# Kernel optimization log

Measured on AMD Instinct MI355X. Metric: run time of the kernel, lower is better.

The kernel has to match this reference:

```python
import jax, jax.numpy as jnp
import numpy as np

B, S, E, H = 2, 2048, 1024, 16
D = E // H  # head dim = 64


def setup_inputs() -> dict:
    key = jax.random.key(0)
    k1, k2, k3 = jax.random.split(key, 3)
    x = jax.random.normal(k1, (B, S, E), dtype=jnp.float32)
    W_attn = jax.random.normal(k2, (E, 3 * E), dtype=jnp.float32) * (1.0 / np.sqrt(E))
    b_attn = jnp.zeros((3 * E,), dtype=jnp.float32)
    W_proj = jax.random.normal(k3, (E, E), dtype=jnp.float32) * (1.0 / np.sqrt(E))
    b_proj = jnp.zeros((E,), dtype=jnp.float32)
    return {"x": x, "W_attn": W_attn, "b_attn": b_attn, "W_proj": W_proj, "b_proj": b_proj}


def reference(x, W_attn, b_attn, W_proj, b_proj):
    b, s, e = x.shape
    qkv = x @ W_attn + b_attn                      # (B, S, 3E)
    q, k, v = jnp.split(qkv, 3, axis=-1)
    # (B, S, E) -> (B, H, S, D)
    def heads(t):
        return t.reshape(b, s, H, D).transpose(0, 2, 1, 3)
    q, k, v = heads(q), heads(k), heads(v)
    scale = 1.0 / np.sqrt(D)
    # ring QK^T over world_size=1 == full QK^T; scores (B, H, S, S)
    attn = jnp.einsum("bhqd,bhkd->bhqk", q, k) * scale
    causal = jnp.tril(jnp.ones((s, s), dtype=bool))
    attn = jnp.where(causal[None, None], attn, -jnp.inf)
    attn = jax.nn.softmax(attn, axis=-1)
    # ring AV over world_size=1 == full AV
    y = jnp.einsum("bhqk,bhkd->bhqd", attn, v)     # (B, H, S, D)
    y = y.transpose(0, 2, 1, 3).reshape(b, s, e)   # (B, S, E)
    return y @ W_proj + b_proj
```

## Files before the change

### kernel.cpp

```cpp
#include <hip/hip_runtime.h>
#include <hip/hip_bf16.h>

#define B_ 2
#define S_ 2048
#define E_ 1024
#define H_ 16
#define D_ 64

typedef __attribute__((ext_vector_type(8))) _Float16 half8;
typedef __attribute__((ext_vector_type(4))) _Float16 half4;
typedef __attribute__((ext_vector_type(4))) float floatx4;

__device__ inline void gload16(const _Float16* g, _Float16* l) {
    __builtin_amdgcn_global_load_lds(
        (const __attribute__((address_space(1))) void*)g,
        (__attribute__((address_space(3))) void*)l, 16, 0, 0);
}

__global__ __launch_bounds__(256) void k_cvt(const float* __restrict__ in,
                                             _Float16* __restrict__ out, int n) {
    int i = (blockIdx.x * 256 + threadIdx.x) * 8;
    if (i >= n) return;
    float4 a = *(const float4*)(in + i);
    float4 b = *(const float4*)(in + i + 4);
    half8 o;
    o[0] = (_Float16)a.x; o[1] = (_Float16)a.y; o[2] = (_Float16)a.z; o[3] = (_Float16)a.w;
    o[4] = (_Float16)b.x; o[5] = (_Float16)b.y; o[6] = (_Float16)b.z; o[7] = (_Float16)b.w;
    *(half8*)(out + i) = o;
}

__global__ __launch_bounds__(256) void k_transpose_cvt(const float* __restrict__ in,
                                                       _Float16* __restrict__ out, int R, int C) {
    __shared__ _Float16 tile[32][33];
    int tx = threadIdx.x & 31, ty = threadIdx.x >> 5;
    int c0 = blockIdx.x * 32, r0 = blockIdx.y * 32;
#pragma unroll
    for (int k = 0; k < 4; k++) {
        int r = ty + k * 8;
        tile[r][tx] = (_Float16)in[(size_t)(r0 + r) * C + c0 + tx];
    }
    __syncthreads();
#pragma unroll
    for (int k = 0; k < 4; k++) {
        int r = ty + k * 8;
        out[(size_t)(c0 + r) * R + r0 + tx] = tile[tx][r];
    }
}

template <int MODE>
__global__ __launch_bounds__(256) void k_gemm(const _Float16* __restrict__ A,
                                              const _Float16* __restrict__ Bt,
                                              const float* __restrict__ bias,
                                              void* __restrict__ out0,
                                              _Float16* __restrict__ out1,
                                              _Float16* __restrict__ out2,
                                              int M, int N, int K) {
    __shared__ __align__(16) _Float16 As[128 * 32];
    __shared__ __align__(16) _Float16 Bs[128 * 32];
    int tid = threadIdx.x;
    int lane = tid & 63, w = tid >> 6;
    int wm = w >> 1, wn = w & 1;
    int l15 = lane & 15, quad = lane >> 4;
    int m0 = blockIdx.y * 128, n0 = blockIdx.x * 128;

    floatx4 acc[4][4];
    floatx4 zero = {0.f, 0.f, 0.f, 0.f};
#pragma unroll
    for (int i = 0; i < 4; i++)
#pragma unroll
        for (int j = 0; j < 4; j++) acc[i][j] = zero;

    for (int k0 = 0; k0 < K; k0 += 32) {
        __syncthreads();
#pragma unroll
        for (int c = 0; c < 2; c++) {
            int flat = c * 2048 + tid * 8;
            int row = flat >> 5, col = flat & 31;
            gload16(A + (size_t)(m0 + row) * K + k0 + col, &As[c * 2048 + w * 512]);
            gload16(Bt + (size_t)(n0 + row) * K + k0 + col, &Bs[c * 2048 + w * 512]);
        }
        __syncthreads();
        half8 af[4], bfr[4];
#pragma unroll
        for (int i = 0; i < 4; i++) af[i] = *(const half8*)&As[(wm * 64 + i * 16 + l15) * 32 + quad * 8];
#pragma unroll
        for (int j = 0; j < 4; j++) bfr[j] = *(const half8*)&Bs[(wn * 64 + j * 16 + l15) * 32 + quad * 8];
#pragma unroll
        for (int i = 0; i < 4; i++)
#pragma unroll
            for (int j = 0; j < 4; j++)
                acc[i][j] = __builtin_amdgcn_mfma_f32_16x16x32_f16(af[i], bfr[j], acc[i][j], 0, 0, 0);
    }
#pragma unroll
    for (int j = 0; j < 4; j++) {
        int gcol = n0 + wn * 64 + j * 16 + l15;
        float bj = bias[gcol];
        int sect = gcol >> 10, e = gcol & 1023;
        int hh = e >> 6, dd = e & 63;
#pragma unroll
        for (int i = 0; i < 4; i++) {
            int grow = m0 + wm * 64 + i * 16 + quad * 4;
#pragma unroll
            for (int r = 0; r < 4; r++) {
                float v = acc[i][j][r] + bj;
                if (MODE == 1) {
                    ((float*)out0)[(size_t)(grow + r) * N + gcol] = v;
                } else {
                    int row = grow + r;
                    int bb = row >> 11, ss = row & 2047;
                    size_t hb = (size_t)(bb * H_ + hh);
                    _Float16 v16 = (_Float16)v;
                    if (sect == 0)
                        ((_Float16*)out0)[(hb * S_ + ss) * D_ + dd] = v16;
                    else if (sect == 1)
                        out1[(hb * S_ + ss) * D_ + dd] = v16;
                    else
                        out2[(hb * D_ + dd) * S_ + ss] = v16;
                }
            }
        }
    }
}

__global__ __launch_bounds__(256) __attribute__((amdgpu_waves_per_eu(2, 4)))
void k_attn(const _Float16* __restrict__ Qh,
            const _Float16* __restrict__ Kh,
            const _Float16* __restrict__ Vt,
            _Float16* __restrict__ y) {
    __shared__ __align__(16) _Float16 smem_h[25600];
    int tid = threadIdx.x;
    int lane = tid & 63, w = tid >> 6;
    int l15 = lane & 15, quad = lane >> 4;
    _Float16* KsB = smem_h;
    _Float16* VsB = smem_h + 8192;
    _Float16* Pw = smem_h + 16384 + w * 2304;

    int bidx = blockIdx.x;
    int bh = 4 * (bidx & 7) + ((bidx >> 3) & 3);
    int qidx = (bidx >> 5) & 7;
    int qb = (bidx >> 8) ? qidx : (15 - qidx);
    int b = bh >> 4, h = bh & 15;

    const size_t hbase = (size_t)bh * (S_ * D_);
    const _Float16* Qp = Qh + hbase;
    const _Float16* Kp = Kh + hbase;
    const _Float16* Vp = Vt + hbase;

    int q0w = qb * 128 + 32 * w;
    int ktd = q0w >> 6;
    int ktmax = 2 * qb + 1;

    int r0 = tid >> 3;
    int cbh = ((tid * 8) & 63) ^ ((r0 & 7) << 3);
    const _Float16* kS0 = Kp + (size_t)r0 * D_ + cbh;
    const _Float16* kS1 = Kp + (size_t)(r0 + 32) * D_ + cbh;
    const _Float16* vS0 = Vp + (size_t)r0 * S_ + cbh;
    const _Float16* vS1 = Vp + (size_t)(r0 + 32) * S_ + cbh;

#define STAGE(kt_, buf_)                                              \
    do {                                                              \
        gload16(kS0 + (kt_) * 4096, KsB + (buf_) * 4096 + w * 512);   \
        gload16(kS1 + (kt_) * 4096, KsB + (buf_) * 4096 + 2048 + w * 512); \
        gload16(vS0 + (kt_) * 64, VsB + (buf_) * 4096 + w * 512);     \
        gload16(vS1 + (kt_) * 64, VsB + (buf_) * 4096 + 2048 + w * 512); \
    } while (0)

    half8 aq[2][2];
#pragma unroll
    for (int i = 0; i < 2; i++)
#pragma unroll
        for (int kk = 0; kk < 2; kk++) {
            half8 q = *(const half8*)(Qp + (size_t)(q0w + i * 16 + l15) * D_ + kk * 32 + quad * 8);
#pragma unroll
            for (int u = 0; u < 8; u++) q[u] *= (_Float16)0.125f;
            aq[i][kk] = q;
        }

    floatx4 zero = {0.f, 0.f, 0.f, 0.f};
    floatx4 o[2][4];
#pragma unroll
    for (int i = 0; i < 2; i++)
#pragma unroll
        for (int f = 0; f < 4; f++) o[i][f] = zero;
    float l_run[2] = {0.f, 0.f};

    STAGE(0, 0);
    int cur = 0;
    int swz = (l15 & 7) << 3;
    for (int kt = 0; kt <= ktmax; kt++) {
        __syncthreads();
        if (kt < ktmax) STAGE(kt + 1, cur ^ 1);
        if (kt <= ktd) {
            const _Float16* KC = KsB + cur * 4096;
            const _Float16* VC = VsB + cur * 4096;
            floatx4 sa[2][4];
#pragma unroll
            for (int jj = 0; jj < 4; jj++) {
                int row = jj * 16 + l15;
                half8 k0 = *(const half8*)&KC[row * 64 + ((quad * 8) ^ swz)];
                half8 k1 = *(const half8*)&KC[row * 64 + ((32 + quad * 8) ^ swz)];
#pragma unroll
                for (int i = 0; i < 2; i++) {
                    floatx4 a = zero;
                    a = __builtin_amdgcn_mfma_f32_16x16x32_f16(k0, aq[i][0], a, 0, 0, 0);
                    a = __builtin_amdgcn_mfma_f32_16x16x32_f16(k1, aq[i][1], a, 0, 0, 0);
                    sa[i][jj] = a;
                }
            }
            bool diag = (kt == ktd);
            int k64 = kt * 64;
#pragma unroll
            for (int i = 0; i < 2; i++) {
                float ssum = 0.f;
#pragma unroll
                for (int jj = 0; jj < 4; jj++) {
                    half4 pk;
#pragma unroll
                    for (int r = 0; r < 4; r++) {
                        float v = __expf(sa[i][jj][r]);
                        if (diag) {
                            int key = k64 + jj * 16 + quad * 4 + r;
                            int query = q0w + i * 16 + l15;
                            if (key > query) v = 0.f;
                        }
                        ssum += v;
                        pk[r] = (_Float16)v;
                    }
                    *(half4*)&Pw[(i * 16 + l15) * 72 + jj * 16 + quad * 4] = pk;
                }
                ssum += __shfl_xor(ssum, 16);
                ssum += __shfl_xor(ssum, 32);
                l_run[i] += ssum;
            }
#pragma unroll
            for (int kk = 0; kk < 2; kk++) {
                half8 ap0 = *(const half8*)&Pw[(0 * 16 + l15) * 72 + kk * 32 + quad * 8];
                half8 ap1 = *(const half8*)&Pw[(1 * 16 + l15) * 72 + kk * 32 + quad * 8];
#pragma unroll
                for (int f = 0; f < 4; f++) {
                    int row = f * 16 + l15;
                    half8 bv = *(const half8*)&VC[row * 64 + ((kk * 32 + quad * 8) ^ swz)];
                    o[0][f] = __builtin_amdgcn_mfma_f32_16x16x32_f16(ap0, bv, o[0][f], 0, 0, 0);
                    o[1][f] = __builtin_amdgcn_mfma_f32_16x16x32_f16(ap1, bv, o[1][f], 0, 0, 0);
                }
            }
        }
        cur ^= 1;
    }
#undef STAGE

#pragma unroll
    for (int i = 0; i < 2; i++) {
        float linv[4];
#pragma unroll
        for (int r = 0; r < 4; r++) linv[r] = 1.0f / __shfl(l_run[i], quad * 4 + r);
#pragma unroll
        for (int f = 0; f < 4; f++)
#pragma unroll
            for (int r = 0; r < 4; r++) {
                int row = q0w + i * 16 + quad * 4 + r;
                y[((size_t)(b * S_ + row)) * E_ + h * D_ + f * 16 + l15] =
                    (_Float16)(o[i][f][r] * linv[r]);
            }
    }
}

extern "C" void kernel_launch(void* const* d_in, const int* in_sizes, int n_in,
                              void* d_out, int out_size, void* d_ws, size_t ws_size,
                              hipStream_t stream) {
    const float* x      = (const float*)d_in[0];
    const float* W_attn = (const float*)d_in[1];
    const float* b_attn = (const float*)d_in[2];
    const float* W_proj = (const float*)d_in[3];
    const float* b_proj = (const float*)d_in[4];
    float* out = (float*)d_out;

    const int M = B_ * S_;
    char* ws = (char*)d_ws;
    _Float16* xh  = (_Float16*)ws; ws += (size_t)M * E_ * 2;
    _Float16* Wat = (_Float16*)ws; ws += (size_t)3 * E_ * E_ * 2;
    _Float16* Wpt = (_Float16*)ws; ws += (size_t)E_ * E_ * 2;
    _Float16* Qh  = (_Float16*)ws; ws += (size_t)M * E_ * 2;
    _Float16* Kh  = (_Float16*)ws; ws += (size_t)M * E_ * 2;
    _Float16* Vt  = (_Float16*)ws; ws += (size_t)M * E_ * 2;
    _Float16* yh  = xh;

    k_cvt<<<(M * E_) / 2048, 256, 0, stream>>>(x, xh, M * E_);
    k_transpose_cvt<<<dim3(3 * E_ / 32, E_ / 32), 256, 0, stream>>>(W_attn, Wat, E_, 3 * E_);
    k_transpose_cvt<<<dim3(E_ / 32, E_ / 32), 256, 0, stream>>>(W_proj, Wpt, E_, E_);

    k_gemm<0><<<dim3(3 * E_ / 128, M / 128), 256, 0, stream>>>(xh, Wat, b_attn, Qh, Kh, Vt, M, 3 * E_, E_);
    k_attn<<<512, 256, 0, stream>>>(Qh, Kh, Vt, yh);
    k_gemm<1><<<dim3(E_ / 128, M / 128), 256, 0, stream>>>(yh, Wpt, b_proj, (void*)out, nullptr, nullptr, M, E_, E_);
}
```

Before: 201.9 us.

## Use 8 waves per attention block and merge prep conversions into one kernel

```diff
diff --git a/kernel.cpp b/kernel.cpp
--- a/kernel.cpp
+++ b/kernel.cpp
@@ -17,23 +17,35 @@
         (__attribute__((address_space(3))) void*)l, 16, 0, 0);
 }
 
-__global__ __launch_bounds__(256) void k_cvt(const float* __restrict__ in,
-                                             _Float16* __restrict__ out, int n) {
-    int i = (blockIdx.x * 256 + threadIdx.x) * 8;
-    if (i >= n) return;
-    float4 a = *(const float4*)(in + i);
-    float4 b = *(const float4*)(in + i + 4);
-    half8 o;
-    o[0] = (_Float16)a.x; o[1] = (_Float16)a.y; o[2] = (_Float16)a.z; o[3] = (_Float16)a.w;
-    o[4] = (_Float16)b.x; o[5] = (_Float16)b.y; o[6] = (_Float16)b.z; o[7] = (_Float16)b.w;
-    *(half8*)(out + i) = o;
-}
-
-__global__ __launch_bounds__(256) void k_transpose_cvt(const float* __restrict__ in,
-                                                       _Float16* __restrict__ out, int R, int C) {
+__global__ __launch_bounds__(256) void k_prep(const float* __restrict__ x, _Float16* __restrict__ xh,
+                                              const float* __restrict__ Wa, _Float16* __restrict__ Wat,
+                                              const float* __restrict__ Wp, _Float16* __restrict__ Wpt) {
     __shared__ _Float16 tile[32][33];
-    int tx = threadIdx.x & 31, ty = threadIdx.x >> 5;
-    int c0 = blockIdx.x * 32, r0 = blockIdx.y * 32;
+    int bid = blockIdx.x, tid = threadIdx.x;
+    if (bid < 2048) {
+        int i = (bid * 256 + tid) * 8;
+        float4 a = *(const float4*)(x + i);
+        float4 b = *(const float4*)(x + i + 4);
+        half8 o;
+        o[0] = (_Float16)a.x; o[1] = (_Float16)a.y; o[2] = (_Float16)a.z; o[3] = (_Float16)a.w;
+        o[4] = (_Float16)b.x; o[5] = (_Float16)b.y; o[6] = (_Float16)b.z; o[7] = (_Float16)b.w;
+        *(half8*)(xh + i) = o;
+        return;
+    }
+    const float* in;
+    _Float16* out;
+    int R, C, bx, by;
+    if (bid < 5120) {
+        int t = bid - 2048;
+        in = Wa; out = Wat; R = E_; C = 3 * E_;
+        bx = t % 96; by = t / 96;
+    } else {
+        int t = bid - 5120;
+        in = Wp; out = Wpt; R = E_; C = E_;
+        bx = t & 31; by = t >> 5;
+    }
+    int tx = tid & 31, ty = tid >> 5;
+    int c0 = bx * 32, r0 = by * 32;
 #pragma unroll
     for (int k = 0; k < 4; k++) {
         int r = ty + k * 8;
@@ -122,7 +134,7 @@
     }
 }
 
-__global__ __launch_bounds__(256) __attribute__((amdgpu_waves_per_eu(2, 4)))
+__global__ __launch_bounds__(512, 4)
 void k_attn(const _Float16* __restrict__ Qh,
             const _Float16* __restrict__ Kh,
             const _Float16* __restrict__ Vt,
@@ -133,7 +145,7 @@
     int l15 = lane & 15, quad = lane >> 4;
     _Float16* KsB = smem_h;
     _Float16* VsB = smem_h + 8192;
-    _Float16* Pw = smem_h + 16384 + w * 2304;
+    _Float16* Pw = smem_h + 16384 + w * (16 * 72);
 
     int bidx = blockIdx.x;
     int bh = 4 * (bidx & 7) + ((bidx >> 3) & 3);
@@ -146,43 +158,35 @@
     const _Float16* Kp = Kh + hbase;
     const _Float16* Vp = Vt + hbase;
 
-    int q0w = qb * 128 + 32 * w;
+    int q0w = qb * 128 + 16 * w;
     int ktd = q0w >> 6;
     int ktmax = 2 * qb + 1;
 
     int r0 = tid >> 3;
     int cbh = ((tid * 8) & 63) ^ ((r0 & 7) << 3);
-    const _Float16* kS0 = Kp + (size_t)r0 * D_ + cbh;
-    const _Float16* kS1 = Kp + (size_t)(r0 + 32) * D_ + cbh;
-    const _Float16* vS0 = Vp + (size_t)r0 * S_ + cbh;
-    const _Float16* vS1 = Vp + (size_t)(r0 + 32) * S_ + cbh;
-
-#define STAGE(kt_, buf_)                                              \
-    do {                                                              \
-        gload16(kS0 + (kt_) * 4096, KsB + (buf_) * 4096 + w * 512);   \
-        gload16(kS1 + (kt_) * 4096, KsB + (buf_) * 4096 + 2048 + w * 512); \
-        gload16(vS0 + (kt_) * 64, VsB + (buf_) * 4096 + w * 512);     \
-        gload16(vS1 + (kt_) * 64, VsB + (buf_) * 4096 + 2048 + w * 512); \
+    const _Float16* kS = Kp + (size_t)r0 * D_ + cbh;
+    const _Float16* vS = Vp + (size_t)r0 * S_ + cbh;
+
+#define STAGE(kt_, buf_)                                             \
+    do {                                                             \
+        gload16(kS + (size_t)(kt_) * 4096, KsB + (buf_) * 4096 + w * 512); \
+        gload16(vS + (size_t)(kt_) * 64, VsB + (buf_) * 4096 + w * 512);   \
     } while (0)
 
-    half8 aq[2][2];
-#pragma unroll
-    for (int i = 0; i < 2; i++)
-#pragma unroll
-        for (int kk = 0; kk < 2; kk++) {
-            half8 q = *(const half8*)(Qp + (size_t)(q0w + i * 16 + l15) * D_ + kk * 32 + quad * 8);
-#pragma unroll
-            for (int u = 0; u < 8; u++) q[u] *= (_Float16)0.125f;
-            aq[i][kk] = q;
-        }
+    half8 aq[2];
+#pragma unroll
+    for (int kk = 0; kk < 2; kk++) {
+        half8 q = *(const half8*)(Qp + (size_t)(q0w + l15) * D_ + kk * 32 + quad * 8);
+#pragma unroll
+        for (int u = 0; u < 8; u++) q[u] *= (_Float16)0.125f;
+        aq[kk] = q;
+    }
 
     floatx4 zero = {0.f, 0.f, 0.f, 0.f};
-    floatx4 o[2][4];
-#pragma unroll
-    for (int i = 0; i < 2; i++)
-#pragma unroll
-        for (int f = 0; f < 4; f++) o[i][f] = zero;
-    float l_run[2] = {0.f, 0.f};
+    floatx4 o[4];
+#pragma unroll
+    for (int f = 0; f < 4; f++) o[f] = zero;
+    float l_run = 0.f;
 
     STAGE(0, 0);
     int cur = 0;
@@ -193,55 +197,47 @@
         if (kt <= ktd) {
             const _Float16* KC = KsB + cur * 4096;
             const _Float16* VC = VsB + cur * 4096;
-            floatx4 sa[2][4];
+            floatx4 sa[4];
 #pragma unroll
             for (int jj = 0; jj < 4; jj++) {
                 int row = jj * 16 + l15;
                 half8 k0 = *(const half8*)&KC[row * 64 + ((quad * 8) ^ swz)];
                 half8 k1 = *(const half8*)&KC[row * 64 + ((32 + quad * 8) ^ swz)];
-#pragma unroll
-                for (int i = 0; i < 2; i++) {
-                    floatx4 a = zero;
-                    a = __builtin_amdgcn_mfma_f32_16x16x32_f16(k0, aq[i][0], a, 0, 0, 0);
-                    a = __builtin_amdgcn_mfma_f32_16x16x32_f16(k1, aq[i][1], a, 0, 0, 0);
-                    sa[i][jj] = a;
-                }
+                floatx4 a = zero;
+                a = __builtin_amdgcn_mfma_f32_16x16x32_f16(k0, aq[0], a, 0, 0, 0);
+                a = __builtin_amdgcn_mfma_f32_16x16x32_f16(k1, aq[1], a, 0, 0, 0);
+                sa[jj] = a;
             }
             bool diag = (kt == ktd);
             int k64 = kt * 64;
-#pragma unroll
-            for (int i = 0; i < 2; i++) {
-                float ssum = 0.f;
-#pragma unroll
-                for (int jj = 0; jj < 4; jj++) {
-                    half4 pk;
-#pragma unroll
-                    for (int r = 0; r < 4; r++) {
-                        float v = __expf(sa[i][jj][r]);
-                        if (diag) {
-                            int key = k64 + jj * 16 + quad * 4 + r;
-                            int query = q0w + i * 16 + l15;
-                            if (key > query) v = 0.f;
-                        }
-                        ssum += v;
-                        pk[r] = (_Float16)v;
+            float ssum = 0.f;
+#pragma unroll
+            for (int jj = 0; jj < 4; jj++) {
+                half4 pk;
+#pragma unroll
+                for (int r = 0; r < 4; r++) {
+                    float v = __expf(sa[jj][r]);
+                    if (diag) {
+                        int key = k64 + jj * 16 + quad * 4 + r;
+                        int query = q0w + l15;
+                        if (key > query) v = 0.f;
                     }
-                    *(half4*)&Pw[(i * 16 + l15) * 72 + jj * 16 + quad * 4] = pk;
+                    ssum += v;
+                    pk[r] = (_Float16)v;
                 }
-                ssum += __shfl_xor(ssum, 16);
-                ssum += __shfl_xor(ssum, 32);
-                l_run[i] += ssum;
-            }
+                *(half4*)&Pw[l15 * 72 + jj * 16 + quad * 4] = pk;
+            }
+            ssum += __shfl_xor(ssum, 16);
+            ssum += __shfl_xor(ssum, 32);
+            l_run += ssum;
 #pragma unroll
             for (int kk = 0; kk < 2; kk++) {
-                half8 ap0 = *(const half8*)&Pw[(0 * 16 + l15) * 72 + kk * 32 + quad * 8];
-                half8 ap1 = *(const half8*)&Pw[(1 * 16 + l15) * 72 + kk * 32 + quad * 8];
+                half8 ap = *(const half8*)&Pw[l15 * 72 + kk * 32 + quad * 8];
 #pragma unroll
                 for (int f = 0; f < 4; f++) {
                     int row = f * 16 + l15;
                     half8 bv = *(const half8*)&VC[row * 64 + ((kk * 32 + quad * 8) ^ swz)];
-                    o[0][f] = __builtin_amdgcn_mfma_f32_16x16x32_f16(ap0, bv, o[0][f], 0, 0, 0);
-                    o[1][f] = __builtin_amdgcn_mfma_f32_16x16x32_f16(ap1, bv, o[1][f], 0, 0, 0);
+                    o[f] = __builtin_amdgcn_mfma_f32_16x16x32_f16(ap, bv, o[f], 0, 0, 0);
                 }
             }
         }
@@ -249,20 +245,17 @@
     }
 #undef STAGE
 
-#pragma unroll
-    for (int i = 0; i < 2; i++) {
-        float linv[4];
-#pragma unroll
-        for (int r = 0; r < 4; r++) linv[r] = 1.0f / __shfl(l_run[i], quad * 4 + r);
-#pragma unroll
-        for (int f = 0; f < 4; f++)
-#pragma unroll
-            for (int r = 0; r < 4; r++) {
-                int row = q0w + i * 16 + quad * 4 + r;
-                y[((size_t)(b * S_ + row)) * E_ + h * D_ + f * 16 + l15] =
-                    (_Float16)(o[i][f][r] * linv[r]);
-            }
-    }
+    float linv[4];
+#pragma unroll
+    for (int r = 0; r < 4; r++) linv[r] = 1.0f / __shfl(l_run, quad * 4 + r);
+#pragma unroll
+    for (int f = 0; f < 4; f++)
+#pragma unroll
+        for (int r = 0; r < 4; r++) {
+            int row = q0w + quad * 4 + r;
+            y[((size_t)(b * S_ + row)) * E_ + h * D_ + f * 16 + l15] =
+                (_Float16)(o[f][r] * linv[r]);
+        }
 }
 
 extern "C" void kernel_launch(void* const* d_in, const int* in_sizes, int n_in,
@@ -285,11 +278,8 @@
     _Float16* Vt  = (_Float16*)ws; ws += (size_t)M * E_ * 2;
     _Float16* yh  = xh;
 
-    k_cvt<<<(M * E_) / 2048, 256, 0, stream>>>(x, xh, M * E_);
-    k_transpose_cvt<<<dim3(3 * E_ / 32, E_ / 32), 256, 0, stream>>>(W_attn, Wat, E_, 3 * E_);
-    k_transpose_cvt<<<dim3(E_ / 32, E_ / 32), 256, 0, stream>>>(W_proj, Wpt, E_, E_);
-
+    k_prep<<<6144, 256, 0, stream>>>(x, xh, W_attn, Wat, W_proj, Wpt);
     k_gemm<0><<<dim3(3 * E_ / 128, M / 128), 256, 0, stream>>>(xh, Wat, b_attn, Qh, Kh, Vt, M, 3 * E_, E_);
-    k_attn<<<512, 256, 0, stream>>>(Qh, Kh, Vt, yh);
+    k_attn<<<512, 512, 0, stream>>>(Qh, Kh, Vt, yh);
     k_gemm<1><<<dim3(E_ / 128, M / 128), 256, 0, stream>>>(yh, Wpt, b_proj, (void*)out, nullptr, nullptr, M, E_, E_);
 }
```

Result: faster. 193.8 us (-4.0%).
